# Kernel tuning notes

Measured on AMD Instinct MI355X. Metric: run time of the kernel, lower is better.

The kernel has to match this reference:

```python
import jax, jax.numpy as jnp
import numpy as np

B = 32768          # batch
H = 512            # hidden_size (SPINN encode dim)
MD = 8             # meta_embed_dim (pinned: 5*(MD-4)==20)
CD = 1024          # classifier_dim
MV = 1000          # meta vocab size
NCAT = 262144      # total ragged category ids (~8 per example)
EPS = 1e-6


def setup_inputs() -> dict:
    key = jax.random.key(0)
    ks = jax.random.split(key, 16)
    return {
        "encode": jax.random.normal(ks[0], (B, H), dtype=jnp.float32),
        "credit_vec": jax.random.uniform(ks[1], (B, 6), dtype=jnp.float32),
        "meta_table": jax.random.normal(ks[2], (MV, MD), dtype=jnp.float32),
        "conv_w": jax.random.normal(ks[3], (5, 6, 3), dtype=jnp.float32) * 0.1,
        "conv_b": jax.random.normal(ks[4], (5,), dtype=jnp.float32) * 0.1,
        "ln1_g": jnp.ones((H + 20,), dtype=jnp.float32),
        "ln1_b": jnp.zeros((H + 20,), dtype=jnp.float32),
        "mlp1_w": jax.random.normal(ks[5], (CD, H + 20), dtype=jnp.float32) * (2.0 / (H + 20)) ** 0.5,
        "mlp1_b": jax.random.normal(ks[6], (CD,), dtype=jnp.float32) * 0.01,
        "ln2_g": jnp.ones((CD,), dtype=jnp.float32),
        "ln2_b": jnp.zeros((CD,), dtype=jnp.float32),
        "out_w": jax.random.normal(ks[7], (6, CD), dtype=jnp.float32) * (2.0 / CD) ** 0.5,
        "out_b": jax.random.normal(ks[8], (6,), dtype=jnp.float32) * 0.01,
        "meta_ids": jax.random.randint(ks[9], (B, 5), 0, MV, dtype=jnp.int64 if jax.config.jax_enable_x64 else jnp.int32),
        "cat_ids": jax.random.randint(ks[10], (NCAT,), 0, MV, dtype=jnp.int64 if jax.config.jax_enable_x64 else jnp.int32),
        "cat_seg": jnp.sort(jax.random.randint(ks[11], (NCAT,), 0, B, dtype=jnp.int64 if jax.config.jax_enable_x64 else jnp.int32)),
    }


def _layer_norm(x, g, b):
    mu = x.mean(-1, keepdims=True)
    var = jnp.mean((x - mu) ** 2, axis=-1, keepdims=True)
    return g * (x - mu) / jnp.sqrt(var + EPS) + b


def reference(encode, credit_vec, meta_table, conv_w, conv_b, ln1_g, ln1_b,
              mlp1_w, mlp1_b, ln2_g, ln2_b, out_w, out_b,
              meta_ids, cat_ids, cat_seg):
    # --- get_meta_mat: ragged per-example category mean-pool (segment mean) ---
    cat_embeds = meta_table[cat_ids]                                   # [NCAT, MD]
    sums = jax.ops.segment_sum(cat_embeds, cat_seg, num_segments=B)    # [B, MD]
    counts = jax.ops.segment_sum(jnp.ones((cat_ids.shape[0],), cat_embeds.dtype),
                                 cat_seg, num_segments=B)              # [B]
    avg_cat = sums / jnp.maximum(counts, 1.0)[:, None]                 # [B, MD]
    meta_embeds = meta_table[meta_ids]                                 # [B, 5, MD]
    meta_mat = jnp.concatenate([avg_cat[:, None, :], meta_embeds], axis=1)  # [B, 6, MD]

    # --- extract_meta_features: Conv1d(6->5,k=3) + ReLU + MaxPool1d(3,1) ---
    conv = jax.lax.conv_general_dilated(meta_mat, conv_w, (1,), 'VALID',
                                        dimension_numbers=('NCH', 'OIH', 'NCH'))
    conv = jax.nn.relu(conv + conv_b[None, :, None])                   # [B, 5, MD-2]
    pooled = jax.lax.reduce_window(conv, -jnp.inf, jax.lax.max,
                                   (1, 1, 3), (1, 1, 1), 'VALID')      # [B, 5, MD-4]
    meta_feat = pooled.reshape(pooled.shape[0], -1)                    # [B, 20]

    # --- build_biases: normalize credit vec, uniform fallback on zero-sum ---
    s = credit_vec.sum(-1, keepdims=True)
    biases = jnp.where(s > 0, credit_vec / s, 1.0 / 6.0)               # [B, 6]
    biases = jax.lax.stop_gradient(biases)  # requires_grad=False in original

    # --- classifier head ---
    mlp_input = jnp.concatenate([encode, meta_feat], axis=-1)          # [B, H+20]
    features = _layer_norm(mlp_input, ln1_g, ln1_b)
    features = jax.nn.relu(features @ mlp1_w.T + mlp1_b)               # [B, CD]
    features = _layer_norm(features, ln2_g, ln2_b)
    output = features @ out_w.T + out_b + biases                       # [B, 6]
    return output
```

## Files before the change

kernel.cpp:

```cpp
#include <hip/hip_runtime.h>

#define BSZ   32768
#define H     512
#define K1DIM 532
#define KPAD  544
#define ASTR  552
#define CD    1024
#define NCATS 262144
#define LNEPS 1e-6f

typedef short bf16x8 __attribute__((ext_vector_type(8)));
typedef float f32x4  __attribute__((ext_vector_type(4)));

__device__ __forceinline__ unsigned short f2bf(float x) {
    unsigned int u = __float_as_uint(x);
    u += 0x7FFFu + ((u >> 16) & 1u);
    return (unsigned short)(u >> 16);
}

__device__ __forceinline__ unsigned int pack_bf2(float lo, float hi) {
    return __builtin_amdgcn_perm(__float_as_uint(hi), __float_as_uint(lo), 0x07060302u);
}

__device__ __forceinline__ float dpp_red16(float x) {
    x += __int_as_float(__builtin_amdgcn_update_dpp(0, __float_as_int(x), 0xB1, 0xf, 0xf, true));
    x += __int_as_float(__builtin_amdgcn_update_dpp(0, __float_as_int(x), 0x4E, 0xf, 0xf, true));
    x += __int_as_float(__builtin_amdgcn_update_dpp(0, __float_as_int(x), 0x114, 0xf, 0xf, true));
    x += __int_as_float(__builtin_amdgcn_update_dpp(0, __float_as_int(x), 0x118, 0xf, 0xf, true));
    return x;
}

__device__ __forceinline__ int psearch64(const int* __restrict__ seg, int target) {
    int lane = threadIdx.x & 63;
    int lo = 0, step = 4096;
    #pragma unroll
    for (int lvl = 0; lvl < 3; ++lvl) {
        int idx = lo + lane * step;
        bool lt = (idx < NCATS) && (seg[idx < NCATS ? idx : NCATS - 1] < target);
        unsigned long long m = __ballot(lt);
        int c = __popcll(m);
        if (c > 0) lo = lo + (c - 1) * step + 1;
        step >>= 6;
    }
    return lo;
}

__global__ void k_prep(const float* __restrict__ w1f, const float* __restrict__ ln1_g,
                       const float* __restrict__ ln1_b, const float* __restrict__ ln2_g,
                       const float* __restrict__ ln2_b, const float* __restrict__ out_w,
                       const float* __restrict__ out_b,
                       unsigned short* __restrict__ w1b, float* __restrict__ G,
                       float* __restrict__ B0, float* __restrict__ c0, float* __restrict__ c1) {
    const int bid = blockIdx.x, tid = threadIdx.x;
    if (bid < 2176) {
        int idx = bid * 256 + tid;
        int row = idx / KPAD, k = idx - row * KPAD;
        float v = (k < K1DIM) ? w1f[(size_t)row * K1DIM + k] * ln1_g[k] : 0.f;
        w1b[idx] = f2bf(v);
    } else if (bid < 2432) {
        int col = (bid - 2176) * 4 + (tid >> 6);
        int lane = tid & 63;
        float g = 0.f, b = 0.f;
        for (int k = lane; k < K1DIM; k += 64) {
            float wv = w1f[(size_t)col * K1DIM + k];
            g = fmaf(ln1_g[k], wv, g);
            b = fmaf(ln1_b[k], wv, b);
        }
        for (int m = 1; m < 64; m <<= 1) { g += __shfl_xor(g, m); b += __shfl_xor(b, m); }
        if (lane == 0) { G[col] = g; B0[col] = b; }
    } else {
        int j = tid >> 5, lane = tid & 31;
        if (j < 6) {
            float s1 = 0.f, s0 = 0.f;
            for (int c = lane; c < CD; c += 32) {
                float w = out_w[j * CD + c];
                s1 = fmaf(ln2_g[c], w, s1);
                s0 = fmaf(ln2_b[c], w, s0);
            }
            for (int m = 1; m < 32; m <<= 1) { s1 += __shfl_xor(s1, m); s0 += __shfl_xor(s0, m); }
            if (lane == 0) { c1[j] = s1; c0[j] = s0 + out_b[j]; }
        }
    }
}

__global__ __launch_bounds__(512, 2) void k_mainw(
    const float* __restrict__ encode, const float* __restrict__ credit,
    const float* __restrict__ meta_table, const float* __restrict__ conv_w,
    const float* __restrict__ conv_b,
    const unsigned short* __restrict__ w1b, const float* __restrict__ b1,
    const float* __restrict__ ln2_g, const float* __restrict__ out_w,
    const float* __restrict__ Gc, const float* __restrict__ B0c,
    const float* __restrict__ c0p, const float* __restrict__ c1p,
    const int* __restrict__ meta_ids, const int* __restrict__ cat_ids,
    const int* __restrict__ cat_seg, float* __restrict__ out)
{
    __shared__ unsigned short Alds[64 * ASTR];
    __shared__ float Sbuf[64][8][8];
    __shared__ float cwL[90], cbL[5];
    __shared__ float sEnc[64], qEnc[64];
    __shared__ float muL[64], rsL[64];
    __shared__ float mu2[64], rs2[64];
    __shared__ float c0L[6], c1L[6];
    __shared__ int   startsL[65];
    __shared__ int   sLoL, sHiL;

    const int tid  = threadIdx.x;
    const int row0 = blockIdx.x * 64;
    const int lane = tid & 63;
    const int w    = tid >> 6;

    if (w == 0) {
        int L = psearch64(cat_seg, row0);
        if (lane == 0) sLoL = L;
    } else if (w == 1) {
        int L = psearch64(cat_seg, row0 + 64);
        if (lane == 0) sHiL = L;
    } else {
        const int t = tid - 128;
        if (t < 90) cwL[t] = conv_w[t];
        else if (t < 95) cbL[t - 90] = conv_b[t - 90];
        else if (t < 101) c0L[t - 95] = c0p[t - 95];
        else if (t < 107) c1L[t - 101] = c1p[t - 101];
    }
    __syncthreads();

    {
        const int slo = sLoL, shi = sHiL;
        for (int i = slo - 1 + tid; i < shi; i += 512) {
            int a = (i >= 0) ? cat_seg[i] : -1;
            int b = (i + 1 < NCATS) ? cat_seg[i + 1] : BSZ;
            int rlo = max(a + 1, row0);
            int rhi = min(b, row0 + 64);
            for (int r = rlo; r <= rhi; ++r) startsL[r - row0] = i + 1;
        }
    }
    __syncthreads();

    {
        const int r = tid >> 3, k = tid & 7;
        const int s = startsL[r], e = startsL[r + 1];
        float sum[8];
        #pragma unroll
        for (int d = 0; d < 8; d++) sum[d] = 0.f;
        for (int i = s + k; i < e; i += 8) {
            int id = cat_ids[i];
            const float4 a = *(const float4*)(meta_table + (size_t)id * 8);
            const float4 b = *(const float4*)(meta_table + (size_t)id * 8 + 4);
            sum[0] += a.x; sum[1] += a.y; sum[2] += a.z; sum[3] += a.w;
            sum[4] += b.x; sum[5] += b.y; sum[6] += b.z; sum[7] += b.w;
        }
        #pragma unroll
        for (int m = 1; m <= 4; m <<= 1)
            #pragma unroll
            for (int d = 0; d < 8; d++) sum[d] += __shfl_xor(sum[d], m);
        if (k == 0) {
            float inv = 1.f / fmaxf((float)(e - s), 1.f);
            #pragma unroll
            for (int d = 0; d < 8; d++) Sbuf[r][0][d] = sum[d] * inv;
        } else if (k <= 5) {
            int id = meta_ids[(size_t)(row0 + r) * 5 + (k - 1)];
            const float4 a = *(const float4*)(meta_table + (size_t)id * 8);
            const float4 b = *(const float4*)(meta_table + (size_t)id * 8 + 4);
            Sbuf[r][k][0] = a.x; Sbuf[r][k][1] = a.y; Sbuf[r][k][2] = a.z; Sbuf[r][k][3] = a.w;
            Sbuf[r][k][4] = b.x; Sbuf[r][k][5] = b.y; Sbuf[r][k][6] = b.z; Sbuf[r][k][7] = b.w;
        }
    }
    __syncthreads();

    if (tid < 64) {
        const int r = tid;
        float mm[6][8];
        #pragma unroll
        for (int ic = 0; ic < 6; ic++)
            #pragma unroll
            for (int d = 0; d < 8; d++) mm[ic][d] = Sbuf[r][ic][d];
        float mfv[20];
        #pragma unroll
        for (int oc = 0; oc < 5; oc++) {
            float c[6];
            #pragma unroll
            for (int x = 0; x < 6; x++) {
                float a = cbL[oc];
                #pragma unroll
                for (int ic = 0; ic < 6; ic++)
                    #pragma unroll
                    for (int k = 0; k < 3; k++)
                        a = fmaf(mm[ic][x + k], cwL[(oc * 6 + ic) * 3 + k], a);
                c[x] = fmaxf(a, 0.f);
            }
            #pragma unroll
            for (int x = 0; x < 4; x++)
                mfv[oc * 4 + x] = fmaxf(fmaxf(c[x], c[x + 1]), c[x + 2]);
        }
        float s = 0.f, q = 0.f;
        unsigned short* arow = Alds + r * ASTR;
        #pragma unroll
        for (int j = 0; j < 20; j++) {
            s += mfv[j]; q = fmaf(mfv[j], mfv[j], q);
            arow[512 + j] = f2bf(mfv[j]);
        }
        #pragma unroll
        for (int t = 0; t < 12; t++) arow[532 + t] = 0;
        sEnc[r] = s; qEnc[r] = q;
    }
    __syncthreads();

    {
        const int r  = tid >> 3;
        const int cl = tid & 7;
        const float* erow = encode + (size_t)(row0 + r) * H;
        unsigned short* arow = Alds + r * ASTR;
        float s = 0.f, q = 0.f;
        #pragma unroll 4
        for (int i = 0; i < 16; i++) {
            int col = cl * 4 + i * 32;
            const float4 v = *(const float4*)(erow + col);
            s += v.x + v.y + v.z + v.w;
            q += v.x*v.x + v.y*v.y + v.z*v.z + v.w*v.w;
            ushort4 st = { f2bf(v.x), f2bf(v.y), f2bf(v.z), f2bf(v.w) };
            *(ushort4*)(arow + col) = st;
        }
        #pragma unroll
        for (int m = 1; m <= 4; m <<= 1) { s += __shfl_xor(s, m); q += __shfl_xor(q, m); }
        if (cl == 0) { sEnc[r] += s; qEnc[r] += q; }
    }
    __syncthreads();
    if (tid < 64) {
        float mean = sEnc[tid] * (1.f / K1DIM);
        float var  = qEnc[tid] * (1.f / K1DIM) - mean * mean;
        muL[tid] = mean;
        rsL[tid] = rsqrtf(var + LNEPS);
    }
    __syncthreads();

    const int ln   = lane & 15;
    const int quad = lane >> 4;
    const int cb   = w * 128;
    const unsigned short* aBase = Alds + ln * ASTR + quad * 8;
    const unsigned short* bp0   = w1b + (size_t)(cb + ln) * KPAD + quad * 8;

#define LDA(A, kk) { _Pragma("unroll") for (int rt = 0; rt < 4; rt++) \
        A[rt] = *(const bf16x8*)(aBase + rt * 16 * ASTR + (kk) * 32); }
#define LDB8(Bv, kk) { _Pragma("unroll") for (int ct = 0; ct < 8; ct++) \
        Bv[ct] = *(const bf16x8*)(bp0 + (size_t)ct * 16 * KPAD + (kk) * 32); }
#define MFM(A, Bv) { _Pragma("unroll") for (int ct = 0; ct < 8; ct++) \
        _Pragma("unroll") for (int rt = 0; rt < 4; rt++) \
        acc[rt][ct] = __builtin_amdgcn_mfma_f32_16x16x32_bf16(A[rt], Bv[ct], acc[rt][ct], 0, 0, 0); }

    f32x4 acc[4][8];
    #pragma unroll
    for (int rt = 0; rt < 4; rt++)
        #pragma unroll
        for (int ct = 0; ct < 8; ct++)
            acc[rt][ct] = f32x4{0.f, 0.f, 0.f, 0.f};

    bf16x8 bP[8], bQ[8], aF[4], aG[4];
    LDB8(bP, 0)
    LDB8(bQ, 1)
    #pragma unroll 1
    for (int kk = 0; kk < 16; kk += 2) {
        LDA(aF, kk)
        MFM(aF, bP)
        LDB8(bP, kk + 2)
        LDA(aG, kk + 1)
        MFM(aG, bQ)
        int k3 = (kk + 3 <= 16) ? kk + 3 : 1;
        LDB8(bQ, k3)
    }
    LDA(aF, 16)
    MFM(aF, bP)
#undef LDA
#undef LDB8
#undef MFM

    int colc[8]; float Gv[8], Bv[8], bv[8], vv[6][8];
    #pragma unroll
    for (int ct = 0; ct < 8; ct++) {
        colc[ct] = cb + ct * 16 + ln;
        Gv[ct] = Gc[colc[ct]]; Bv[ct] = B0c[colc[ct]]; bv[ct] = b1[colc[ct]];
        float g2 = ln2_g[colc[ct]];
        #pragma unroll
        for (int j = 0; j < 6; j++) vv[j][ct] = g2 * out_w[j * CD + colc[ct]];
    }
    #pragma unroll
    for (int rt = 0; rt < 4; rt++) {
        #pragma unroll
        for (int reg = 0; reg < 4; reg++) {
            const int row = rt * 16 + quad * 4 + reg;
            const float mu = muL[row], rs = rsL[row];
            float s = 0.f, q = 0.f, p[6];
            #pragma unroll
            for (int j = 0; j < 6; j++) p[j] = 0.f;
            #pragma unroll
            for (int ct = 0; ct < 8; ct++) {
                float h = fmaxf(rs * (acc[rt][ct][reg] - mu * Gv[ct]) + Bv[ct] + bv[ct], 0.f);
                s += h; q = fmaf(h, h, q);
                #pragma unroll
                for (int j = 0; j < 6; j++) p[j] = fmaf(h, vv[j][ct], p[j]);
            }
            s = dpp_red16(s); q = dpp_red16(q);
            #pragma unroll
            for (int j = 0; j < 6; j++) p[j] = dpp_red16(p[j]);
            if (ln == 15) {
                float4 lo = { s, q, p[0], p[1] };
                float4 hi = { p[2], p[3], p[4], p[5] };
                *(float4*)&Sbuf[row][w][0] = lo;
                *(float4*)&Sbuf[row][w][4] = hi;
            }
        }
    }
    __syncthreads();

    if (tid < 64) {
        float s = 0.f, q = 0.f;
        #pragma unroll
        for (int ww = 0; ww < 8; ww++) { s += Sbuf[tid][ww][0]; q += Sbuf[tid][ww][1]; }
        float mean = s * (1.f / CD);
        float var  = q * (1.f / CD) - mean * mean;
        mu2[tid] = mean; rs2[tid] = rsqrtf(var + LNEPS);
    }
    __syncthreads();

    if (tid < 384) {
        int r = tid / 6, j = tid - r * 6;
        float S = 0.f;
        #pragma unroll
        for (int ww = 0; ww < 8; ww++) S += Sbuf[r][ww][2 + j];
        int gr = row0 + r;
        float cs = 0.f;
        #pragma unroll
        for (int jj = 0; jj < 6; jj++) cs += credit[(size_t)gr * 6 + jj];
        float bias = (cs > 0.f) ? credit[(size_t)gr * 6 + j] / cs : (1.f / 6.f);
        out[(size_t)gr * 6 + j] = rs2[r] * S - mu2[r] * rs2[r] * c1L[j] + c0L[j] + bias;
    }
}

__global__ __launch_bounds__(512, 2) void k_legacy(
    const float* __restrict__ encode, const float* __restrict__ credit,
    const float* __restrict__ meta_table, const float* __restrict__ conv_w,
    const float* __restrict__ conv_b, const float* __restrict__ ln1_g,
    const float* __restrict__ ln1_b, const float* __restrict__ w1f,
    const float* __restrict__ b1,
    const float* __restrict__ ln2_g, const float* __restrict__ ln2_b,
    const float* __restrict__ out_w, const float* __restrict__ out_b,
    const int* __restrict__ meta_ids, const int* __restrict__ cat_ids,
    const int* __restrict__ cat_seg, float* __restrict__ out)
{
    __shared__ unsigned short Alds[64 * ASTR];
    __shared__ float Vlds[6 * CD];
    __shared__ float gL[K1DIM], bL[K1DIM];
    __shared__ float cwL[90], cbL[5];
    __shared__ float mfL[64][20];
    __shared__ float sEnc[64], qEnc[64];
    __shared__ float muL[64], rsL[64];
    __shared__ float rowsum[64][8], rowsq[64][8];
    __shared__ float mu2[64], rs2[64];
    __shared__ float Sbuf[64][6][8];
    __shared__ float c0L[6], c1L[6];
    __shared__ int   startsL[65];
    __shared__ int   sLoL, sHiL;

    const int tid  = threadIdx.x;
    const int row0 = blockIdx.x * 64;
    const int lane = tid & 63;
    const int w    = tid >> 6;

    if (w == 0) {
        if (lane < 2) {
            int target = row0 + lane * 64;
            int lo = 0, hi = NCATS;
            while (lo < hi) { int mid = (lo + hi) >> 1; if (cat_seg[mid] < target) lo = mid + 1; else hi = mid; }
            if (lane == 0) sLoL = lo; else sHiL = lo;
        }
    } else {
        const int t = tid - 64;
        for (int i = t; i < 6 * CD; i += 448) Vlds[i] = ln2_g[i & (CD - 1)] * out_w[i];
        for (int i = t; i < K1DIM; i += 448) { gL[i] = ln1_g[i]; bL[i] = ln1_b[i]; }
        if (t < 90) cwL[t] = conv_w[t];
        if (t < 5)  cbL[t] = conv_b[t];
        for (int r = w - 1; r < 64; r += 7) {
            const float* p = encode + (size_t)(row0 + r) * H + lane * 8;
            float4 v0 = *(const float4*)p;
            float4 v1 = *(const float4*)(p + 4);
            float s = v0.x + v0.y + v0.z + v0.w + v1.x + v1.y + v1.z + v1.w;
            float q = v0.x*v0.x + v0.y*v0.y + v0.z*v0.z + v0.w*v0.w
                    + v1.x*v1.x + v1.y*v1.y + v1.z*v1.z + v1.w*v1.w;
            for (int m = 1; m < 64; m <<= 1) { s += __shfl_xor(s, m); q += __shfl_xor(q, m); }
            if (lane == 0) { sEnc[r] = s; qEnc[r] = q; }
        }
    }
    __syncthreads();

    {
        const int slo = sLoL, shi = sHiL;
        for (int i = slo - 1 + tid; i < shi; i += 512) {
            int a = (i >= 0) ? cat_seg[i] : -1;
            int b = (i + 1 < NCATS) ? cat_seg[i + 1] : BSZ;
            int rlo = max(a + 1, row0);
            int rhi = min(b, row0 + 64);
            for (int r = rlo; r <= rhi; ++r) startsL[r - row0] = i + 1;
        }
    }
    if (w >= 1 && w <= 6) {
        int j = w - 1;
        float s1 = 0.f, s0 = 0.f;
        for (int c = lane; c < CD; c += 64) {
            s1 += Vlds[j * CD + c];
            s0 = fmaf(ln2_b[c], out_w[j * CD + c], s0);
        }
        for (int m = 1; m < 64; m <<= 1) { s1 += __shfl_xor(s1, m); s0 += __shfl_xor(s0, m); }
        if (lane == 0) { c1L[j] = s1; c0L[j] = s0 + out_b[j]; }
    }
    __syncthreads();

    if (tid < 64) {
        const int r = tid;
        const int s = startsL[r], e = startsL[r + 1];
        float mm[6][8];
        float sum[8];
        #pragma unroll
        for (int d = 0; d < 8; d++) sum[d] = 0.f;
        for (int i = s; i < e; i++) {
            int id = cat_ids[i];
            const float4 a = *(const float4*)(meta_table + (size_t)id * 8);
            const float4 b = *(const float4*)(meta_table + (size_t)id * 8 + 4);
            sum[0] += a.x; sum[1] += a.y; sum[2] += a.z; sum[3] += a.w;
            sum[4] += b.x; sum[5] += b.y; sum[6] += b.z; sum[7] += b.w;
        }
        float cnt = fmaxf((float)(e - s), 1.f);
        #pragma unroll
        for (int d = 0; d < 8; d++) mm[0][d] = sum[d] / cnt;
        #pragma unroll
        for (int i = 0; i < 5; i++) {
            int id = meta_ids[(size_t)(row0 + r) * 5 + i];
            const float4 a = *(const float4*)(meta_table + (size_t)id * 8);
            const float4 b = *(const float4*)(meta_table + (size_t)id * 8 + 4);
            mm[1+i][0] = a.x; mm[1+i][1] = a.y; mm[1+i][2] = a.z; mm[1+i][3] = a.w;
            mm[1+i][4] = b.x; mm[1+i][5] = b.y; mm[1+i][6] = b.z; mm[1+i][7] = b.w;
        }
        float mfv[20];
        #pragma unroll
        for (int oc = 0; oc < 5; oc++) {
            float c[6];
            #pragma unroll
            for (int x = 0; x < 6; x++) {
                float a = cbL[oc];
                #pragma unroll
                for (int ic = 0; ic < 6; ic++)
                    #pragma unroll
                    for (int k = 0; k < 3; k++)
                        a = fmaf(mm[ic][x + k], cwL[(oc * 6 + ic) * 3 + k], a);
                c[x] = fmaxf(a, 0.f);
            }
            #pragma unroll
            for (int x = 0; x < 4; x++)
                mfv[oc * 4 + x] = fmaxf(fmaxf(c[x], c[x + 1]), c[x + 2]);
        }
        float sT = sEnc[r], qT = qEnc[r];
        #pragma unroll
        for (int j = 0; j < 20; j++) {
            mfL[r][j] = mfv[j];
            sT += mfv[j]; qT = fmaf(mfv[j], mfv[j], qT);
        }
        float mean = sT * (1.f / K1DIM);
        float var  = qT * (1.f / K1DIM) - mean * mean;
        muL[r] = mean;
        rsL[r] = rsqrtf(var + LNEPS);
    }
    __syncthreads();

    for (int i = tid; i < 64 * 136; i += 512) {
        int r = i / 136, c4 = i - r * 136;
        int col = c4 * 4;
        unsigned short o0 = 0, o1 = 0, o2 = 0, o3 = 0;
        if (c4 < 133) {
            float x0, x1, x2, x3;
            if (c4 < 128) {
                const float4 v = *(const float4*)&encode[(size_t)(row0 + r) * H + col];
                x0 = v.x; x1 = v.y; x2 = v.z; x3 = v.w;
            } else {
                int o = col - H;
                x0 = mfL[r][o]; x1 = mfL[r][o + 1]; x2 = mfL[r][o + 2]; x3 = mfL[r][o + 3];
            }
            float m = muL[r], rr = rsL[r];
            o0 = f2bf((x0 - m) * rr * gL[col + 0] + bL[col + 0]);
            o1 = f2bf((x1 - m) * rr * gL[col + 1] + bL[col + 1]);
            o2 = f2bf((x2 - m) * rr * gL[col + 2] + bL[col + 2]);
            o3 = f2bf((x3 - m) * rr * gL[col + 3] + bL[col + 3]);
        }
        ushort4 st = { o0, o1, o2, o3 };
        *(ushort4*)&Alds[r * ASTR + col] = st;
    }
    __syncthreads();

    const int ln   = lane & 15;
    const int quad = lane >> 4;
    const int cb   = w * 128;

    f32x4 acc[4][8];
    #pragma unroll
    for (int rt = 0; rt < 4; rt++)
        #pragma unroll
        for (int ct = 0; ct < 8; ct++)
            acc[rt][ct] = f32x4{0.f, 0.f, 0.f, 0.f};

    #pragma unroll 1
    for (int kk = 0; kk < 16; kk++) {
        bf16x8 af[4];
        #pragma unroll
        for (int rt = 0; rt < 4; rt++)
            af[rt] = *(const bf16x8*)&Alds[(rt * 16 + ln) * ASTR + kk * 32 + quad * 8];
        #pragma unroll
        for (int ct = 0; ct < 8; ct++) {
            const float* wrow = w1f + (size_t)(cb + ct * 16 + ln) * K1DIM + kk * 32 + quad * 8;
            const float4 fa = *(const float4*)wrow;
            const float4 fb = *(const float4*)(wrow + 4);
            union { bf16x8 v; unsigned int u[4]; } bu;
            bu.u[0] = pack_bf2(fa.x, fa.y);
            bu.u[1] = pack_bf2(fa.z, fa.w);
            bu.u[2] = pack_bf2(fb.x, fb.y);
            bu.u[3] = pack_bf2(fb.z, fb.w);
            #pragma unroll
            for (int rt = 0; rt < 4; rt++)
                acc[rt][ct] = __builtin_amdgcn_mfma_f32_16x16x32_bf16(af[rt], bu.v, acc[rt][ct], 0, 0, 0);
        }
    }
    {
        bf16x8 af[4];
        #pragma unroll
        for (int rt = 0; rt < 4; rt++)
            af[rt] = *(const bf16x8*)&Alds[(rt * 16 + ln) * ASTR + 512 + quad * 8];
        #pragma unroll
        for (int ct = 0; ct < 8; ct++) {
            union { bf16x8 v; unsigned int u[4]; } bu;
            bu.u[0] = 0; bu.u[1] = 0; bu.u[2] = 0; bu.u[3] = 0;
            const float* wrow = w1f + (size_t)(cb + ct * 16 + ln) * K1DIM + 512 + quad * 8;
            if (quad < 2) {
                const float4 fa = *(const float4*)wrow;
                const float4 fb = *(const float4*)(wrow + 4);
                bu.u[0] = pack_bf2(fa.x, fa.y);
                bu.u[1] = pack_bf2(fa.z, fa.w);
                bu.u[2] = pack_bf2(fb.x, fb.y);
                bu.u[3] = pack_bf2(fb.z, fb.w);
            } else if (quad == 2) {
                const float4 fa = *(const float4*)wrow;
                bu.u[0] = pack_bf2(fa.x, fa.y);
                bu.u[1] = pack_bf2(fa.z, fa.w);
            }
            #pragma unroll
            for (int rt = 0; rt < 4; rt++)
                acc[rt][ct] = __builtin_amdgcn_mfma_f32_16x16x32_bf16(af[rt], bu.v, acc[rt][ct], 0, 0, 0);
        }
    }

    float b1v[8]; int colc[8];
    #pragma unroll
    for (int ct = 0; ct < 8; ct++) { colc[ct] = cb + ct * 16 + ln; b1v[ct] = b1[colc[ct]]; }
    #pragma unroll
    for (int rt = 0; rt < 4; rt++)
        #pragma unroll
        for (int ct = 0; ct < 8; ct++)
            #pragma unroll
            for (int reg = 0; reg < 4; reg++)
                acc[rt][ct][reg] = fmaxf(acc[rt][ct][reg] + b1v[ct], 0.f);

    #pragma unroll
    for (int rt = 0; rt < 4; rt++) {
        #pragma unroll
        for (int reg = 0; reg < 4; reg++) {
            float s = 0.f, q = 0.f;
            #pragma unroll
            for (int ct = 0; ct < 8; ct++) { float f = acc[rt][ct][reg]; s += f; q = fmaf(f, f, q); }
            #pragma unroll
            for (int m = 1; m <= 8; m <<= 1) { s += __shfl_xor(s, m); q += __shfl_xor(q, m); }
            if (ln == 0) {
                int row = rt * 16 + quad * 4 + reg;
                rowsum[row][w] = s; rowsq[row][w] = q;
            }
        }
    }
    __syncthreads();
    if (tid < 64) {
        float s = 0.f, q = 0.f;
        #pragma unroll
        for (int ww = 0; ww < 8; ww++) { s += rowsum[tid][ww]; q += rowsq[tid][ww]; }
        float mean = s * (1.f / CD);
        float var  = q * (1.f / CD) - mean * mean;
        mu2[tid] = mean; rs2[tid] = rsqrtf(var + LNEPS);
    }

    float vv[6][8];
    #pragma unroll
    for (int j = 0; j < 6; j++)
        #pragma unroll
        for (int ct = 0; ct < 8; ct++)
            vv[j][ct] = Vlds[j * CD + colc[ct]];
    #pragma unroll
    for (int rt = 0; rt < 4; rt++) {
        #pragma unroll
        for (int reg = 0; reg < 4; reg++) {
            float p0 = 0.f, p1 = 0.f, p2 = 0.f, p3 = 0.f, p4 = 0.f, p5 = 0.f;
            #pragma unroll
            for (int ct = 0; ct < 8; ct++) {
                float f = acc[rt][ct][reg];
                p0 = fmaf(f, vv[0][ct], p0); p1 = fmaf(f, vv[1][ct], p1);
                p2 = fmaf(f, vv[2][ct], p2); p3 = fmaf(f, vv[3][ct], p3);
                p4 = fmaf(f, vv[4][ct], p4); p5 = fmaf(f, vv[5][ct], p5);
            }
            #pragma unroll
            for (int m = 1; m <= 8; m <<= 1) {
                p0 += __shfl_xor(p0, m); p1 += __shfl_xor(p1, m); p2 += __shfl_xor(p2, m);
                p3 += __shfl_xor(p3, m); p4 += __shfl_xor(p4, m); p5 += __shfl_xor(p5, m);
            }
            if (ln == 0) {
                int row = rt * 16 + quad * 4 + reg;
                Sbuf[row][0][w] = p0; Sbuf[row][1][w] = p1; Sbuf[row][2][w] = p2;
                Sbuf[row][3][w] = p3; Sbuf[row][4][w] = p4; Sbuf[row][5][w] = p5;
            }
        }
    }
    __syncthreads();

    if (tid < 384) {
        int r = tid / 6, j = tid - r * 6;
        float S = 0.f;
        #pragma unroll
        for (int ww = 0; ww < 8; ww++) S += Sbuf[r][j][ww];
        int gr = row0 + r;
        float cs = 0.f;
        #pragma unroll
        for (int jj = 0; jj < 6; jj++) cs += credit[(size_t)gr * 6 + jj];
        float bias = (cs > 0.f) ? credit[(size_t)gr * 6 + j] / cs : (1.f / 6.f);
        out[(size_t)gr * 6 + j] = rs2[r] * S - mu2[r] * rs2[r] * c1L[j] + c0L[j] + bias;
    }
}

extern "C" void kernel_launch(void* const* d_in, const int* in_sizes, int n_in,
                              void* d_out, int out_size, void* d_ws, size_t ws_size,
                              hipStream_t stream) {
    const float* encode     = (const float*)d_in[0];
    const float* credit     = (const float*)d_in[1];
    const float* meta_table = (const float*)d_in[2];
    const float* conv_w     = (const float*)d_in[3];
    const float* conv_b     = (const float*)d_in[4];
    const float* ln1_g      = (const float*)d_in[5];
    const float* ln1_b      = (const float*)d_in[6];
    const float* mlp1_w     = (const float*)d_in[7];
    const float* mlp1_b     = (const float*)d_in[8];
    const float* ln2_g      = (const float*)d_in[9];
    const float* ln2_b      = (const float*)d_in[10];
    const float* out_w      = (const float*)d_in[11];
    const float* out_b      = (const float*)d_in[12];
    const int*   meta_ids   = (const int*)d_in[13];
    const int*   cat_ids    = (const int*)d_in[14];
    const int*   cat_seg    = (const int*)d_in[15];
    float* out = (float*)d_out;

    const size_t OFF_G  = (size_t)CD * KPAD * sizeof(unsigned short);
    const size_t OFF_B0 = OFF_G + CD * sizeof(float);
    const size_t OFF_C0 = OFF_B0 + CD * sizeof(float);
    const size_t OFF_C1 = OFF_C0 + 32;
    const size_t WS_NEED = OFF_C1 + 32;

    if (ws_size >= WS_NEED) {
        char* ws = (char*)d_ws;
        unsigned short* w1b = (unsigned short*)ws;
        float* G  = (float*)(ws + OFF_G);
        float* B0 = (float*)(ws + OFF_B0);
        float* c0 = (float*)(ws + OFF_C0);
        float* c1 = (float*)(ws + OFF_C1);
        k_prep<<<2433, 256, 0, stream>>>(mlp1_w, ln1_g, ln1_b, ln2_g, ln2_b, out_w, out_b,
                                         w1b, G, B0, c0, c1);
        k_mainw<<<BSZ / 64, 512, 0, stream>>>(
            encode, credit, meta_table, conv_w, conv_b,
            w1b, mlp1_b, ln2_g, out_w, G, B0, c0, c1,
            meta_ids, cat_ids, cat_seg, out);
    } else {
        k_legacy<<<BSZ / 64, 512, 0, stream>>>(
            encode, credit, meta_table, conv_w, conv_b, ln1_g, ln1_b,
            mlp1_w, mlp1_b, ln2_g, ln2_b, out_w, out_b,
            meta_ids, cat_ids, cat_seg, out);
    }
}
```

Measured before the change: 204.4 us.

## Split GEMM into two column passes to raise occupancy and fuse meta conv stages

Raises the launch bound from 2 to 4 blocks per CU. To fit, each wave now computes 64 columns per pass over two passes instead of 128 columns at once, which halves the accumulator registers, and drops the second A fragment buffer. Per-row LayerNorm and output partial sums now go into a small shared buffer through LDS atomics, replacing the per-wave Sbuf. The meta gather, conv and maxpool stages are fused into one phase using shuffles, with the encode load moved earlier, which removes several barriers and shrinks LDS. The cost is that the A tile is read from LDS twice, there is LDS atomic contention, and float summation order becomes nondeterministic.

```diff
diff --git a/kernel.cpp b/kernel.cpp
--- a/kernel.cpp
+++ b/kernel.cpp
@@ -83,7 +83,7 @@
     }
 }
 
-__global__ __launch_bounds__(512, 2) void k_mainw(
+__global__ __launch_bounds__(512, 4) void k_mainw(
     const float* __restrict__ encode, const float* __restrict__ credit,
     const float* __restrict__ meta_table, const float* __restrict__ conv_w,
     const float* __restrict__ conv_b,
@@ -95,10 +95,9 @@
     const int* __restrict__ cat_seg, float* __restrict__ out)
 {
     __shared__ unsigned short Alds[64 * ASTR];
-    __shared__ float Sbuf[64][8][8];
+    __shared__ float Ssum[64][10];
     __shared__ float cwL[90], cbL[5];
     __shared__ float sEnc[64], qEnc[64];
-    __shared__ float muL[64], rsL[64];
     __shared__ float mu2[64], rs2[64];
     __shared__ float c0L[6], c1L[6];
     __shared__ int   startsL[65];
@@ -122,6 +121,7 @@
         else if (t < 101) c0L[t - 95] = c0p[t - 95];
         else if (t < 107) c1L[t - 101] = c1p[t - 101];
     }
+    for (int i = tid; i < 640; i += 512) ((float*)Ssum)[i] = 0.f;
     __syncthreads();
 
     {
@@ -134,77 +134,6 @@
             for (int r = rlo; r <= rhi; ++r) startsL[r - row0] = i + 1;
         }
     }
-    __syncthreads();
-
-    {
-        const int r = tid >> 3, k = tid & 7;
-        const int s = startsL[r], e = startsL[r + 1];
-        float sum[8];
-        #pragma unroll
-        for (int d = 0; d < 8; d++) sum[d] = 0.f;
-        for (int i = s + k; i < e; i += 8) {
-            int id = cat_ids[i];
-            const float4 a = *(const float4*)(meta_table + (size_t)id * 8);
-            const float4 b = *(const float4*)(meta_table + (size_t)id * 8 + 4);
-            sum[0] += a.x; sum[1] += a.y; sum[2] += a.z; sum[3] += a.w;
-            sum[4] += b.x; sum[5] += b.y; sum[6] += b.z; sum[7] += b.w;
-        }
-        #pragma unroll
-        for (int m = 1; m <= 4; m <<= 1)
-            #pragma unroll
-            for (int d = 0; d < 8; d++) sum[d] += __shfl_xor(sum[d], m);
-        if (k == 0) {
-            float inv = 1.f / fmaxf((float)(e - s), 1.f);
-            #pragma unroll
-            for (int d = 0; d < 8; d++) Sbuf[r][0][d] = sum[d] * inv;
-        } else if (k <= 5) {
-            int id = meta_ids[(size_t)(row0 + r) * 5 + (k - 1)];
-            const float4 a = *(const float4*)(meta_table + (size_t)id * 8);
-            const float4 b = *(const float4*)(meta_table + (size_t)id * 8 + 4);
-            Sbuf[r][k][0] = a.x; Sbuf[r][k][1] = a.y; Sbuf[r][k][2] = a.z; Sbuf[r][k][3] = a.w;
-            Sbuf[r][k][4] = b.x; Sbuf[r][k][5] = b.y; Sbuf[r][k][6] = b.z; Sbuf[r][k][7] = b.w;
-        }
-    }
-    __syncthreads();
-
-    if (tid < 64) {
-        const int r = tid;
-        float mm[6][8];
-        #pragma unroll
-        for (int ic = 0; ic < 6; ic++)
-            #pragma unroll
-            for (int d = 0; d < 8; d++) mm[ic][d] = Sbuf[r][ic][d];
-        float mfv[20];
-        #pragma unroll
-        for (int oc = 0; oc < 5; oc++) {
-            float c[6];
-            #pragma unroll
-            for (int x = 0; x < 6; x++) {
-                float a = cbL[oc];
-                #pragma unroll
-                for (int ic = 0; ic < 6; ic++)
-                    #pragma unroll
-                    for (int k = 0; k < 3; k++)
-                        a = fmaf(mm[ic][x + k], cwL[(oc * 6 + ic) * 3 + k], a);
-                c[x] = fmaxf(a, 0.f);
-            }
-            #pragma unroll
-            for (int x = 0; x < 4; x++)
-                mfv[oc * 4 + x] = fmaxf(fmaxf(c[x], c[x + 1]), c[x + 2]);
-        }
-        float s = 0.f, q = 0.f;
-        unsigned short* arow = Alds + r * ASTR;
-        #pragma unroll
-        for (int j = 0; j < 20; j++) {
-            s += mfv[j]; q = fmaf(mfv[j], mfv[j], q);
-            arow[512 + j] = f2bf(mfv[j]);
-        }
-        #pragma unroll
-        for (int t = 0; t < 12; t++) arow[532 + t] = 0;
-        sEnc[r] = s; qEnc[r] = q;
-    }
-    __syncthreads();
-
     {
         const int r  = tid >> 3;
         const int cl = tid & 7;
@@ -222,99 +151,170 @@
         }
         #pragma unroll
         for (int m = 1; m <= 4; m <<= 1) { s += __shfl_xor(s, m); q += __shfl_xor(q, m); }
-        if (cl == 0) { sEnc[r] += s; qEnc[r] += q; }
+        if (cl == 0) { sEnc[r] = s; qEnc[r] = q; }
+    }
+    __syncthreads();
+
+    {
+        const int r = tid >> 3, k = tid & 7;
+        const int s = startsL[r], e = startsL[r + 1];
+        float val[8];
+        #pragma unroll
+        for (int d = 0; d < 8; d++) val[d] = 0.f;
+        for (int i = s + k; i < e; i += 8) {
+            int id = cat_ids[i];
+            const float4 a = *(const float4*)(meta_table + (size_t)id * 8);
+            const float4 b = *(const float4*)(meta_table + (size_t)id * 8 + 4);
+            val[0] += a.x; val[1] += a.y; val[2] += a.z; val[3] += a.w;
+            val[4] += b.x; val[5] += b.y; val[6] += b.z; val[7] += b.w;
+        }
+        #pragma unroll
+        for (int m = 1; m <= 4; m <<= 1)
+            #pragma unroll
+            for (int d = 0; d < 8; d++) val[d] += __shfl_xor(val[d], m);
+        float inv = 1.f / fmaxf((float)(e - s), 1.f);
+        if (k == 0) {
+            #pragma unroll
+            for (int d = 0; d < 8; d++) val[d] *= inv;
+        } else if (k <= 5) {
+            int id = meta_ids[(size_t)(row0 + r) * 5 + (k - 1)];
+            const float4 a = *(const float4*)(meta_table + (size_t)id * 8);
+            const float4 b = *(const float4*)(meta_table + (size_t)id * 8 + 4);
+            val[0] = a.x; val[1] = a.y; val[2] = a.z; val[3] = a.w;
+            val[4] = b.x; val[5] = b.y; val[6] = b.z; val[7] = b.w;
+        }
+        const int base = lane & 56;
+        float mm[6][8];
+        #pragma unroll
+        for (int src = 0; src < 6; src++)
+            #pragma unroll
+            for (int d = 0; d < 8; d++)
+                mm[src][d] = __shfl(val[d], base + src);
+        unsigned short* arow = Alds + r * ASTR;
+        float s2 = 0.f, q2 = 0.f;
+        if (k < 5) {
+            const int oc = k;
+            float c[6];
+            #pragma unroll
+            for (int x = 0; x < 6; x++) {
+                float a = cbL[oc];
+                #pragma unroll
+                for (int ic = 0; ic < 6; ic++)
+                    #pragma unroll
+                    for (int kj = 0; kj < 3; kj++)
+                        a = fmaf(mm[ic][x + kj], cwL[(oc * 6 + ic) * 3 + kj], a);
+                c[x] = fmaxf(a, 0.f);
+            }
+            unsigned short o[4];
+            #pragma unroll
+            for (int x = 0; x < 4; x++) {
+                float p = fmaxf(fmaxf(c[x], c[x + 1]), c[x + 2]);
+                s2 += p; q2 = fmaf(p, p, q2);
+                o[x] = f2bf(p);
+            }
+            ushort4 st = { o[0], o[1], o[2], o[3] };
+            *(ushort4*)(arow + 512 + oc * 4) = st;
+        } else {
+            ushort4 z = { 0, 0, 0, 0 };
+            *(ushort4*)(arow + 532 + (k - 5) * 4) = z;
+        }
+        #pragma unroll
+        for (int m = 1; m <= 4; m <<= 1) { s2 += __shfl_xor(s2, m); q2 += __shfl_xor(q2, m); }
+        if (k == 0) { sEnc[r] += s2; qEnc[r] += q2; }
     }
     __syncthreads();
     if (tid < 64) {
         float mean = sEnc[tid] * (1.f / K1DIM);
         float var  = qEnc[tid] * (1.f / K1DIM) - mean * mean;
-        muL[tid] = mean;
-        rsL[tid] = rsqrtf(var + LNEPS);
+        sEnc[tid] = mean;
+        qEnc[tid] = rsqrtf(var + LNEPS);
     }
     __syncthreads();
 
     const int ln   = lane & 15;
     const int quad = lane >> 4;
-    const int cb   = w * 128;
     const unsigned short* aBase = Alds + ln * ASTR + quad * 8;
-    const unsigned short* bp0   = w1b + (size_t)(cb + ln) * KPAD + quad * 8;
 
 #define LDA(A, kk) { _Pragma("unroll") for (int rt = 0; rt < 4; rt++) \
         A[rt] = *(const bf16x8*)(aBase + rt * 16 * ASTR + (kk) * 32); }
-#define LDB8(Bv, kk) { _Pragma("unroll") for (int ct = 0; ct < 8; ct++) \
+#define LDB4(Bv, kk) { _Pragma("unroll") for (int ct = 0; ct < 4; ct++) \
         Bv[ct] = *(const bf16x8*)(bp0 + (size_t)ct * 16 * KPAD + (kk) * 32); }
-#define MFM(A, Bv) { _Pragma("unroll") for (int ct = 0; ct < 8; ct++) \
+#define MFM(A, Bv) { _Pragma("unroll") for (int ct = 0; ct < 4; ct++) \
         _Pragma("unroll") for (int rt = 0; rt < 4; rt++) \
         acc[rt][ct] = __builtin_amdgcn_mfma_f32_16x16x32_bf16(A[rt], Bv[ct], acc[rt][ct], 0, 0, 0); }
 
-    f32x4 acc[4][8];
-    #pragma unroll
-    for (int rt = 0; rt < 4; rt++)
-        #pragma unroll
-        for (int ct = 0; ct < 8; ct++)
-            acc[rt][ct] = f32x4{0.f, 0.f, 0.f, 0.f};
-
-    bf16x8 bP[8], bQ[8], aF[4], aG[4];
-    LDB8(bP, 0)
-    LDB8(bQ, 1)
     #pragma unroll 1
-    for (int kk = 0; kk < 16; kk += 2) {
-        LDA(aF, kk)
+    for (int pass = 0; pass < 2; ++pass) {
+        const int cb = pass * 512 + w * 64;
+        const unsigned short* bp0 = w1b + (size_t)(cb + ln) * KPAD + quad * 8;
+
+        f32x4 acc[4][4];
+        #pragma unroll
+        for (int rt = 0; rt < 4; rt++)
+            #pragma unroll
+            for (int ct = 0; ct < 4; ct++)
+                acc[rt][ct] = f32x4{0.f, 0.f, 0.f, 0.f};
+
+        bf16x8 bP[4], bQ[4], aF[4];
+        LDB4(bP, 0)
+        LDB4(bQ, 1)
+        #pragma unroll 1
+        for (int kk = 0; kk < 16; kk += 2) {
+            LDA(aF, kk)
+            MFM(aF, bP)
+            LDB4(bP, kk + 2)
+            LDA(aF, kk + 1)
+            MFM(aF, bQ)
+            int k3 = (kk + 3 <= 16) ? kk + 3 : 1;
+            LDB4(bQ, k3)
+        }
+        LDA(aF, 16)
         MFM(aF, bP)
-        LDB8(bP, kk + 2)
-        LDA(aG, kk + 1)
-        MFM(aG, bQ)
-        int k3 = (kk + 3 <= 16) ? kk + 3 : 1;
-        LDB8(bQ, k3)
-    }
-    LDA(aF, 16)
-    MFM(aF, bP)
+
+        int colc[4]; float Gv[4], Bv[4], bv[4], vv[6][4];
+        #pragma unroll
+        for (int ct = 0; ct < 4; ct++) {
+            colc[ct] = cb + ct * 16 + ln;
+            Gv[ct] = Gc[colc[ct]]; Bv[ct] = B0c[colc[ct]]; bv[ct] = b1[colc[ct]];
+            float g2 = ln2_g[colc[ct]];
+            #pragma unroll
+            for (int j = 0; j < 6; j++) vv[j][ct] = g2 * out_w[j * CD + colc[ct]];
+        }
+        #pragma unroll
+        for (int rt = 0; rt < 4; rt++) {
+            #pragma unroll
+            for (int reg = 0; reg < 4; reg++) {
+                const int row = rt * 16 + quad * 4 + reg;
+                const float mu = sEnc[row], rs = qEnc[row];
+                float s = 0.f, q = 0.f, p[6];
+                #pragma unroll
+                for (int j = 0; j < 6; j++) p[j] = 0.f;
+                #pragma unroll
+                for (int ct = 0; ct < 4; ct++) {
+                    float h = fmaxf(rs * (acc[rt][ct][reg] - mu * Gv[ct]) + Bv[ct] + bv[ct], 0.f);
+                    s += h; q = fmaf(h, h, q);
+                    #pragma unroll
+                    for (int j = 0; j < 6; j++) p[j] = fmaf(h, vv[j][ct], p[j]);
+                }
+                s = dpp_red16(s); q = dpp_red16(q);
+                #pragma unroll
+                for (int j = 0; j < 6; j++) p[j] = dpp_red16(p[j]);
+                if (ln == 15) {
+                    atomicAdd(&Ssum[row][0], s);
+                    atomicAdd(&Ssum[row][1], q);
+                    #pragma unroll
+                    for (int j = 0; j < 6; j++) atomicAdd(&Ssum[row][2 + j], p[j]);
+                }
+            }
+        }
+    }
 #undef LDA
-#undef LDB8
+#undef LDB4
 #undef MFM
-
-    int colc[8]; float Gv[8], Bv[8], bv[8], vv[6][8];
-    #pragma unroll
-    for (int ct = 0; ct < 8; ct++) {
-        colc[ct] = cb + ct * 16 + ln;
-        Gv[ct] = Gc[colc[ct]]; Bv[ct] = B0c[colc[ct]]; bv[ct] = b1[colc[ct]];
-        float g2 = ln2_g[colc[ct]];
-        #pragma unroll
-        for (int j = 0; j < 6; j++) vv[j][ct] = g2 * out_w[j * CD + colc[ct]];
-    }
-    #pragma unroll
-    for (int rt = 0; rt < 4; rt++) {
-        #pragma unroll
-        for (int reg = 0; reg < 4; reg++) {
-            const int row = rt * 16 + quad * 4 + reg;
-            const float mu = muL[row], rs = rsL[row];
-            float s = 0.f, q = 0.f, p[6];
-            #pragma unroll
-            for (int j = 0; j < 6; j++) p[j] = 0.f;
-            #pragma unroll
-            for (int ct = 0; ct < 8; ct++) {
-                float h = fmaxf(rs * (acc[rt][ct][reg] - mu * Gv[ct]) + Bv[ct] + bv[ct], 0.f);
-                s += h; q = fmaf(h, h, q);
-                #pragma unroll
-                for (int j = 0; j < 6; j++) p[j] = fmaf(h, vv[j][ct], p[j]);
-            }
-            s = dpp_red16(s); q = dpp_red16(q);
-            #pragma unroll
-            for (int j = 0; j < 6; j++) p[j] = dpp_red16(p[j]);
-            if (ln == 15) {
-                float4 lo = { s, q, p[0], p[1] };
-                float4 hi = { p[2], p[3], p[4], p[5] };
-                *(float4*)&Sbuf[row][w][0] = lo;
-                *(float4*)&Sbuf[row][w][4] = hi;
-            }
-        }
-    }
     __syncthreads();
 
     if (tid < 64) {
-        float s = 0.f, q = 0.f;
-        #pragma unroll
-        for (int ww = 0; ww < 8; ww++) { s += Sbuf[tid][ww][0]; q += Sbuf[tid][ww][1]; }
+        float s = Ssum[tid][0], q = Ssum[tid][1];
         float mean = s * (1.f / CD);
         float var  = q * (1.f / CD) - mean * mean;
         mu2[tid] = mean; rs2[tid] = rsqrtf(var + LNEPS);
@@ -323,9 +323,7 @@
 
     if (tid < 384) {
         int r = tid / 6, j = tid - r * 6;
-        float S = 0.f;
-        #pragma unroll
-        for (int ww = 0; ww < 8; ww++) S += Sbuf[r][ww][2 + j];
+        float S = Ssum[r][2 + j];
         int gr = row0 + r;
         float cs = 0.f;
         #pragma unroll
```

New measurement: 192.1 us. -6.0%, faster.
